# Optimization experiments

Hardware: AMD Instinct MI355X
Metric: run time of the kernel (lower is better)

Reference implementation:

```python
import jax, jax.numpy as jnp
import numpy as np

DIM = 3456      # visual_dim
E = 1024        # embed_dim = dim_head*heads = 128*8
H = 8
D = E // H
LN_EPS = 1e-5


def _mlp(x, w1, b1, w2, b2):
    # nn.Sequential(Linear, GELU(exact), Linear)
    h = jax.nn.gelu(x @ w1.T + b1, approximate=False)
    return h @ w2.T + b2


def _ln(x, g, b):
    m = jnp.mean(x, axis=-1, keepdims=True)
    v = jnp.mean((x - m) ** 2, axis=-1, keepdims=True)
    return (x - m) * jax.lax.rsqrt(v + LN_EPS) * g + b


def setup_inputs() -> dict:
    key = jax.random.key(0)
    ks = jax.random.split(key, 24)
    std = 0.02
    d = {"x": jax.random.normal(ks[0], (5, 729, DIM), dtype=jnp.float32)}
    i = 1
    for name in ("q", "k", "v"):
        d[f"{name}_w1"] = std * jax.random.normal(ks[i], (E, DIM), dtype=jnp.float32); i += 1
        d[f"{name}_b1"] = jnp.zeros((E,), jnp.float32)
        d[f"{name}_w2"] = std * jax.random.normal(ks[i], (E, E), dtype=jnp.float32); i += 1
        d[f"{name}_b2"] = jnp.zeros((E,), jnp.float32)
        d[f"ln_{name}_g"] = jnp.ones((E,), jnp.float32)
        d[f"ln_{name}_b"] = jnp.zeros((E,), jnp.float32)
    d["in_proj_w"] = std * jax.random.normal(ks[i], (3 * E, E), dtype=jnp.float32); i += 1
    d["in_proj_b"] = jnp.zeros((3 * E,), jnp.float32)
    d["out_proj_w"] = std * jax.random.normal(ks[i], (E, E), dtype=jnp.float32); i += 1
    d["out_proj_b"] = jnp.zeros((E,), jnp.float32)
    d["to_out_w"] = std * jax.random.normal(ks[i], (DIM, E), dtype=jnp.float32)
    return d


def reference(x,
              q_w1, q_b1, q_w2, q_b2, ln_q_g, ln_q_b,
              k_w1, k_b1, k_w2, k_b2, ln_k_g, ln_k_b,
              v_w1, v_b1, v_w2, v_b2, ln_v_g, ln_v_b,
              in_proj_w, in_proj_b, out_proj_w, out_proj_b, to_out_w):
    t, hw, c = x.shape
    # spatial_temporal pattern: x_multi = x, no interpolation.
    # q/k/v: MLP -> LN -> permute(1,0,2) -> divide_feature -> flatten.
    # divide_feature is a pure permutation of tokens; all tokens end up in a
    # single (L, 1, E) attention, so full attention over the flattened
    # (hw, t) token order computes the identical result.
    q = _ln(_mlp(x, q_w1, q_b1, q_w2, q_b2), ln_q_g, ln_q_b)  # (t, hw, E)
    k = _ln(_mlp(x, k_w1, k_b1, k_w2, k_b2), ln_k_g, ln_k_b)
    v = _ln(_mlp(x, v_w1, v_b1, v_w2, v_b2), ln_v_g, ln_v_b)
    L = t * hw
    q = q.transpose(1, 0, 2).reshape(L, E)  # (hw*t, E), (h,w,t)-major order
    k = k.transpose(1, 0, 2).reshape(L, E)
    v = v.transpose(1, 0, 2).reshape(L, E)
    # nn.MultiheadAttention with packed in_proj
    qp = (q @ in_proj_w[:E].T + in_proj_b[:E]).reshape(L, H, D)
    kp = (k @ in_proj_w[E:2 * E].T + in_proj_b[E:2 * E]).reshape(L, H, D)
    vp = (v @ in_proj_w[2 * E:].T + in_proj_b[2 * E:]).reshape(L, H, D)
    scale = 1.0 / jnp.sqrt(jnp.asarray(D, q.dtype))
    scores = jnp.einsum('qhd,khd->hqk', qp, kp) * scale  # (H, L, L)
    attn = jax.nn.softmax(scores, axis=-1)
    o = jnp.einsum('hqk,khd->qhd', attn, vp).reshape(L, E)
    o = o @ out_proj_w.T + out_proj_b
    o = o.reshape(hw, t, E).transpose(1, 0, 2)  # (t, hw, E)
    out = o @ to_out_w.T                         # (t, hw, c)
    return x + out
```

## Files before the change

### kernel.cpp

```cpp
#include <hip/hip_runtime.h>
#include <hip/hip_bf16.h>

#define L_TOK 3645
#define MP    3712
#define DIMV  3456
#define EDIM  1024

typedef __attribute__((ext_vector_type(8))) short bf8;
typedef __attribute__((ext_vector_type(4))) short s4v;
typedef __attribute__((ext_vector_type(4))) float f4;

__device__ __forceinline__ short f2b(float f) {
  union { float f; unsigned u; } v; v.f = f;
  unsigned r = v.u + 0x7fffu + ((v.u >> 16) & 1u);
  return (short)(r >> 16);
}
__device__ __forceinline__ float b2f(short s) {
  union { unsigned u; float f; } v; v.u = ((unsigned)(unsigned short)s) << 16;
  return v.f;
}
__device__ __forceinline__ void gld16(const void* g, void* l) {
  __builtin_amdgcn_global_load_lds(
      (const __attribute__((address_space(1))) void*)(unsigned long long)g,
      (__attribute__((address_space(3))) void*)(unsigned)(unsigned long long)l,
      16, 0, 0);
}

__global__ __launch_bounds__(256) void k_cvt(const float* __restrict__ src,
                                             short* __restrict__ dst, int n4) {
  int i = blockIdx.x * 256 + threadIdx.x;
  if (i >= n4) return;
  float4 v = ((const float4*)src)[i];
  s4v o; o[0] = f2b(v.x); o[1] = f2b(v.y); o[2] = f2b(v.z); o[3] = f2b(v.w);
  ((s4v*)dst)[i] = o;
}
__global__ __launch_bounds__(256) void k_cvt_pad(const float* __restrict__ src,
                                                 short* __restrict__ dst, int n4src, int n4tot) {
  int i = blockIdx.x * 256 + threadIdx.x;
  if (i >= n4tot) return;
  s4v o; o[0] = 0; o[1] = 0; o[2] = 0; o[3] = 0;
  if (i < n4src) {
    float4 v = ((const float4*)src)[i];
    o[0] = f2b(v.x); o[1] = f2b(v.y); o[2] = f2b(v.z); o[3] = f2b(v.w);
  }
  ((s4v*)dst)[i] = o;
}

#define GM_GELU   0
#define GM_BIAS   1
#define GM_QSCALE 2
#define GM_RESID  3

template<int MODE>
__global__ __launch_bounds__(256)
void k_gemm(const short* __restrict__ A, long sA,
            const short* __restrict__ B, long sB,
            const float* __restrict__ bias0, const float* __restrict__ bias1,
            const float* __restrict__ bias2,
            void* __restrict__ Cout, long sC,
            int N, int K, const float* __restrict__ resid)
{
  __shared__ short As[2][128 * 32];
  __shared__ short Bs[2][128 * 32];
  const int tid  = threadIdx.x;
  const int z    = blockIdx.z;

  const int nwg  = gridDim.x * gridDim.y;
  const int orig = blockIdx.y * gridDim.x + blockIdx.x;
  const int qq   = nwg >> 3, rr = nwg & 7;
  const int xcd  = orig & 7, ofs = orig >> 3;
  const int swz  = (xcd < rr ? xcd * (qq + 1) : rr * (qq + 1) + (xcd - rr) * qq) + ofs;
  const int brow = (swz / gridDim.x) * 128;
  const int bcol = (swz % gridDim.x) * 128;

  const short* Ab = A + (long)z * sA;
  const short* Bb = B + (long)z * sB;
  const float* bias = (z == 0) ? bias0 : (z == 1 ? bias1 : bias2);

  const int wave = tid >> 6, lane = tid & 63;
  const int lg = lane >> 4, lc = lane & 15;
  const int m0 = (wave >> 1) * 64, n0 = (wave & 1) * 64;

  const int r0 = tid >> 2, seg = tid & 3;
  const int r1 = r0 + 64;
  const int so0 = (seg ^ ((r0 >> 1) & 3)) * 8;
  const int so1 = (seg ^ ((r1 >> 1) & 3)) * 8;
  const short* pA0 = Ab + (long)(brow + r0) * K + so0;
  const short* pA1 = Ab + (long)(brow + r1) * K + so1;
  const short* pB0 = Bb + (long)(bcol + r0) * K + so0;
  const short* pB1 = Bb + (long)(bcol + r1) * K + so1;

  f4 acc[4][4];
  f4 zero = {0.f, 0.f, 0.f, 0.f};
#pragma unroll
  for (int i = 0; i < 4; ++i)
#pragma unroll
    for (int j = 0; j < 4; ++j) acc[i][j] = zero;

  auto STAGE = [&](int buf) {
    gld16(pA0, &As[buf][tid * 8]);
    gld16(pA1, &As[buf][(tid + 256) * 8]);
    gld16(pB0, &Bs[buf][tid * 8]);
    gld16(pB1, &Bs[buf][(tid + 256) * 8]);
    pA0 += 32; pA1 += 32; pB0 += 32; pB1 += 32;
  };

  const int NT = K >> 5;
  STAGE(0);

  for (int t = 0; t < NT; ++t) {
    const int buf = t & 1;
    asm volatile("s_waitcnt vmcnt(0)" ::: "memory");
    __builtin_amdgcn_sched_barrier(0);
    __builtin_amdgcn_s_barrier();
    if (t + 1 < NT) STAGE((t + 1) & 1);

    const short* Al = &As[buf][0];
    const short* Bl = &Bs[buf][0];
    bf8 af[4], bfr[4];
#pragma unroll
    for (int mi = 0; mi < 4; ++mi) {
      int r = m0 + mi * 16 + lc;
      af[mi] = *(const bf8*)&Al[r * 32 + ((lg ^ ((r >> 1) & 3)) * 8)];
    }
#pragma unroll
    for (int ni = 0; ni < 4; ++ni) {
      int r = n0 + ni * 16 + lc;
      bfr[ni] = *(const bf8*)&Bl[r * 32 + ((lg ^ ((r >> 1) & 3)) * 8)];
    }
    __builtin_amdgcn_s_setprio(1);
#pragma unroll
    for (int mi = 0; mi < 4; ++mi)
#pragma unroll
      for (int ni = 0; ni < 4; ++ni)
        acc[mi][ni] = __builtin_amdgcn_mfma_f32_16x16x32_bf16(af[mi], bfr[ni], acc[mi][ni], 0, 0, 0);
    __builtin_amdgcn_s_setprio(0);
    __builtin_amdgcn_sched_barrier(0);
  }

  if (MODE == GM_RESID) {
    float* C = (float*)Cout;
#pragma unroll
    for (int ni = 0; ni < 4; ++ni) {
      int col = bcol + n0 + ni * 16 + lc;
#pragma unroll
      for (int mi = 0; mi < 4; ++mi)
#pragma unroll
        for (int r = 0; r < 4; ++r) {
          int row = brow + m0 + mi * 16 + lg * 4 + r;
          if (row < L_TOK)
            C[(long)row * N + col] = acc[mi][ni][r] + resid[(long)row * N + col];
        }
    }
  } else {
    short* C = (short*)Cout + (long)z * sC;
    const float alpha = (MODE == GM_QSCALE && z == 0) ? 0.08838834764831845f : 1.0f;
#pragma unroll
    for (int ni = 0; ni < 4; ++ni) {
      int col = bcol + n0 + ni * 16 + lc;
      float bv = bias[col];
#pragma unroll
      for (int mi = 0; mi < 4; ++mi)
#pragma unroll
        for (int r = 0; r < 4; ++r) {
          int row = brow + m0 + mi * 16 + lg * 4 + r;
          float v = acc[mi][ni][r] + bv;
          if (MODE == GM_GELU) v = 0.5f * v * (1.f + erff(v * 0.70710678118654752f));
          v *= alpha;
          C[(long)row * EDIM + col] = f2b(v);
        }
    }
  }
}

__global__ __launch_bounds__(256)
void k_ln(const short* __restrict__ A, short* __restrict__ Y,
          const float* __restrict__ g0, const float* __restrict__ g1, const float* __restrict__ g2,
          const float* __restrict__ b0, const float* __restrict__ b1, const float* __restrict__ b2)
{
  const int row = blockIdx.x, z = blockIdx.y;
  const float* g = (z == 0) ? g0 : (z == 1 ? g1 : g2);
  const float* b = (z == 0) ? b0 : (z == 1 ? b1 : b2);
  const short* a = A + ((long)z * MP + row) * EDIM;
  short* y = Y + ((long)z * MP + row) * EDIM;
  const int t = threadIdx.x;
  s4v v = *(const s4v*)&a[t * 4];
  float x0 = b2f(v[0]), x1 = b2f(v[1]), x2 = b2f(v[2]), x3 = b2f(v[3]);
  float s = x0 + x1 + x2 + x3;
  float q = x0 * x0 + x1 * x1 + x2 * x2 + x3 * x3;
#pragma unroll
  for (int off = 1; off < 64; off <<= 1) { s += __shfl_xor(s, off); q += __shfl_xor(q, off); }
  __shared__ float rs[4], rq[4];
  if ((t & 63) == 0) { rs[t >> 6] = s; rq[t >> 6] = q; }
  __syncthreads();
  s = rs[0] + rs[1] + rs[2] + rs[3];
  q = rq[0] + rq[1] + rq[2] + rq[3];
  float mean = s * (1.f / 1024.f);
  float var  = q * (1.f / 1024.f) - mean * mean;
  float rstd = rsqrtf(var + 1e-5f);
  s4v o;
#pragma unroll
  for (int j = 0; j < 4; ++j) {
    int col = t * 4 + j;
    o[j] = f2b((b2f(v[j]) - mean) * rstd * g[col] + b[col]);
  }
  *(s4v*)&y[t * 4] = o;
}

__global__ __launch_bounds__(256)
void k_vtrans(const short* __restrict__ vp, short* __restrict__ vpT)
{
  const int kb = blockIdx.x * 64, h = blockIdx.y;
  __shared__ short T[64 * 128];
  const int tid = threadIdx.x;
#pragma unroll
  for (int i = 0; i < 4; ++i) {
    int c = tid + 256 * i;
    int r = c >> 4, x = c & 15;
    bf8 val = *(const bf8*)&vp[(long)(kb + r) * EDIM + h * 128 + x * 8];
    *(bf8*)&T[r * 128 + ((x ^ (r & 7)) * 8)] = val;
  }
  __syncthreads();
#pragma unroll
  for (int i = 0; i < 4; ++i) {
    int c = tid + 256 * i;
    int dr = c >> 3, x = c & 7;
    short tmp[8];
#pragma unroll
    for (int e = 0; e < 8; ++e) {
      int kv = x * 8 + e;
      tmp[e] = T[kv * 128 + (((dr >> 3) ^ (kv & 7)) << 3) + (dr & 7)];
    }
    *(bf8*)&vpT[((long)h * 128 + dr) * MP + kb + x * 8] = *(bf8*)tmp;
  }
}

__global__ __launch_bounds__(256)
void k_attn(const short* __restrict__ qp, const short* __restrict__ kp,
            const short* __restrict__ vpT, short* __restrict__ o)
{
  const int bx = blockIdx.x;
  const int h = bx & 7, qb = (bx >> 3) * 128;
  const int tid = threadIdx.x, wave = tid >> 6, lane = tid & 63;
  const int lg = lane >> 4, lc = lane & 15;
  __shared__ short Ks[2][64 * 128];
  __shared__ short Vs[2][128 * 64];
  __shared__ short Ps[4][32 * 64];

  const int q0 = qb + wave * 32;
  bf8 qf[2][4];
#pragma unroll
  for (int g = 0; g < 2; ++g)
#pragma unroll
    for (int d4 = 0; d4 < 4; ++d4)
      qf[g][d4] = *(const bf8*)&qp[(long)(q0 + g * 16 + lc) * EDIM + h * 128 + d4 * 32 + lg * 8];

  f4 oacc[2][8];
  f4 zero = {0.f, 0.f, 0.f, 0.f};
#pragma unroll
  for (int g = 0; g < 2; ++g)
#pragma unroll
    for (int dt = 0; dt < 8; ++dt) oacc[g][dt] = zero;
  float lsum0 = 0.f, lsum1 = 0.f;

  auto STAGE = [&](short* ksb, short* vsb, int kb) {
#pragma unroll
    for (int i = 0; i < 4; ++i) {
      int c = tid + 256 * i; int r = c >> 4, x = c & 15;
      gld16(&kp[(long)(kb + r) * EDIM + h * 128 + (x ^ (r & 7)) * 8], &ksb[c * 8]);
    }
#pragma unroll
    for (int i = 0; i < 4; ++i) {
      int c = tid + 256 * i; int dr = c >> 3, x = c & 7;
      gld16(&vpT[((long)h * 128 + dr) * MP + kb + (x ^ (dr & 7)) * 8], &vsb[c * 8]);
    }
  };

  const int NTILE = (L_TOK + 63) / 64;
  STAGE(Ks[0], Vs[0], 0);

  for (int t = 0; t < NTILE; ++t) {
    const int kb = t * 64;
    const short* ksb = Ks[t & 1];
    const short* vsb = Vs[t & 1];
    __builtin_amdgcn_s_barrier();
    if (t + 1 < NTILE) {
      STAGE(Ks[(t + 1) & 1], Vs[(t + 1) & 1], kb + 64);
      asm volatile("s_waitcnt vmcnt(8)" ::: "memory");
    } else {
      asm volatile("s_waitcnt vmcnt(0)" ::: "memory");
    }
    __builtin_amdgcn_sched_barrier(0);
    __builtin_amdgcn_s_barrier();
    __builtin_amdgcn_sched_barrier(0);

#pragma unroll
    for (int s = 0; s < 4; ++s) {
      const int krow = s * 16 + lc;
      bf8 kf[4];
#pragma unroll
      for (int d4 = 0; d4 < 4; ++d4)
        kf[d4] = *(const bf8*)&ksb[krow * 128 + (((d4 * 4 + lg) ^ (krow & 7)) * 8)];
      f4 sa0 = zero, sa1 = zero;
      __builtin_amdgcn_s_setprio(1);
#pragma unroll
      for (int d4 = 0; d4 < 4; ++d4) {
        sa0 = __builtin_amdgcn_mfma_f32_16x16x32_bf16(kf[d4], qf[0][d4], sa0, 0, 0, 0);
        sa1 = __builtin_amdgcn_mfma_f32_16x16x32_bf16(kf[d4], qf[1][d4], sa1, 0, 0, 0);
      }
      __builtin_amdgcn_s_setprio(0);
      const int kvb = kb + s * 16 + lg * 4;
#pragma unroll
      for (int g = 0; g < 2; ++g) {
        f4 sa = g ? sa1 : sa0;
        float p[4];
#pragma unroll
        for (int r = 0; r < 4; ++r) {
          float e = __expf(sa[r]);
          p[r] = (kvb + r < L_TOK) ? e : 0.f;
          if (g) lsum1 += p[r]; else lsum0 += p[r];
        }
        s4v pk; pk[0] = f2b(p[0]); pk[1] = f2b(p[1]); pk[2] = f2b(p[2]); pk[3] = f2b(p[3]);
        *(s4v*)&Ps[wave][(g * 16 + lc) * 64 + ((s * 16 + lg * 4) ^ ((lc & 7) << 3))] = pk;
      }
    }
    bf8 pf[2][2];
#pragma unroll
    for (int g = 0; g < 2; ++g) {
      pf[g][0] = *(const bf8*)&Ps[wave][(g * 16 + lc) * 64 + ((lg * 8) ^ ((lc & 7) << 3))];
      pf[g][1] = *(const bf8*)&Ps[wave][(g * 16 + lc) * 64 + ((32 + lg * 8) ^ ((lc & 7) << 3))];
    }
#pragma unroll
    for (int dt = 0; dt < 8; ++dt) {
      const int vrow = dt * 16 + lc;
      bf8 vf0 = *(const bf8*)&vsb[vrow * 64 + ((lg ^ (vrow & 7)) * 8)];
      bf8 vf1 = *(const bf8*)&vsb[vrow * 64 + (((4 + lg) ^ (vrow & 7)) * 8)];
      __builtin_amdgcn_s_setprio(1);
      oacc[0][dt] = __builtin_amdgcn_mfma_f32_16x16x32_bf16(pf[0][0], vf0, oacc[0][dt], 0, 0, 0);
      oacc[0][dt] = __builtin_amdgcn_mfma_f32_16x16x32_bf16(pf[0][1], vf1, oacc[0][dt], 0, 0, 0);
      oacc[1][dt] = __builtin_amdgcn_mfma_f32_16x16x32_bf16(pf[1][0], vf0, oacc[1][dt], 0, 0, 0);
      oacc[1][dt] = __builtin_amdgcn_mfma_f32_16x16x32_bf16(pf[1][1], vf1, oacc[1][dt], 0, 0, 0);
      __builtin_amdgcn_s_setprio(0);
    }
    __builtin_amdgcn_sched_barrier(0);
  }

  lsum0 += __shfl_xor(lsum0, 16);
  lsum0 += __shfl_xor(lsum0, 32);
  lsum1 += __shfl_xor(lsum1, 16);
  lsum1 += __shfl_xor(lsum1, 32);
#pragma unroll
  for (int g = 0; g < 2; ++g) {
    float ls = g ? lsum1 : lsum0;
    float rinv[4];
#pragma unroll
    for (int r = 0; r < 4; ++r) rinv[r] = 1.f / __shfl(ls, lg * 4 + r);
#pragma unroll
    for (int dt = 0; dt < 8; ++dt)
#pragma unroll
      for (int r = 0; r < 4; ++r) {
        int orow = q0 + g * 16 + lg * 4 + r;
        o[(long)orow * EDIM + h * 128 + dt * 16 + lc] = f2b(oacc[g][dt][r] * rinv[r]);
      }
  }
}

extern "C" void kernel_launch(void* const* d_in, const int* in_sizes, int n_in,
                              void* d_out, int out_size, void* d_ws, size_t ws_size,
                              hipStream_t stream)
{
  const float* x   = (const float*)d_in[0];
  const float* ipb = (const float*)d_in[20];
  const float* opb = (const float*)d_in[22];

  char* ws = (char*)d_ws;
  short* regA = (short*)(ws + 0);
  short* regB = (short*)(ws + 25657344);
  short* w1b  = (short*)(ws + 48463872);
  short* w2b  = (short*)(ws + 69697536);
  short* wpb  = (short*)(ws + 75988992);
  short* wob  = (short*)(ws + 82280448);
  short* wtb  = (short*)(ws + 84377600);
  short* vpT  = (short*)(ws + 91455488);

  short* xb  = regA;
  short* h1  = regB;
  short* aln = regA;
  short* lnq = regB;
  short* proj = regA;
  short* ob  = regB;
  short* o2  = (short*)(ws + 25657344 + 7602176);

  k_cvt_pad<<<12528, 256, 0, stream>>>(x, xb, 3149280, 3207168);
  k_cvt<<<3456, 256, 0, stream>>>((const float*)d_in[1],  w1b,            884736);
  k_cvt<<<3456, 256, 0, stream>>>((const float*)d_in[7],  w1b + 3538944,  884736);
  k_cvt<<<3456, 256, 0, stream>>>((const float*)d_in[13], w1b + 7077888,  884736);
  k_cvt<<<1024, 256, 0, stream>>>((const float*)d_in[3],  w2b,            262144);
  k_cvt<<<1024, 256, 0, stream>>>((const float*)d_in[9],  w2b + 1048576,  262144);
  k_cvt<<<1024, 256, 0, stream>>>((const float*)d_in[15], w2b + 2097152,  262144);
  k_cvt<<<3072, 256, 0, stream>>>((const float*)d_in[19], wpb,            786432);
  k_cvt<<<1024, 256, 0, stream>>>((const float*)d_in[21], wob,            262144);
  k_cvt<<<3456, 256, 0, stream>>>((const float*)d_in[23], wtb,            884736);

  dim3 g3(8, 29, 3), g1(8, 29, 1);
  k_gemm<GM_GELU><<<g3, 256, 0, stream>>>(xb, 0, w1b, 3538944,
      (const float*)d_in[2], (const float*)d_in[8], (const float*)d_in[14],
      h1, (long)MP * EDIM, EDIM, DIMV, nullptr);
  k_gemm<GM_BIAS><<<g3, 256, 0, stream>>>(h1, (long)MP * EDIM, w2b, 1048576,
      (const float*)d_in[4], (const float*)d_in[10], (const float*)d_in[16],
      aln, (long)MP * EDIM, EDIM, EDIM, nullptr);
  dim3 gl(MP, 3);
  k_ln<<<gl, 256, 0, stream>>>(aln, lnq,
      (const float*)d_in[5], (const float*)d_in[11], (const float*)d_in[17],
      (const float*)d_in[6], (const float*)d_in[12], (const float*)d_in[18]);
  k_gemm<GM_QSCALE><<<g3, 256, 0, stream>>>(lnq, (long)MP * EDIM, wpb, 1048576,
      ipb, ipb + 1024, ipb + 2048,
      proj, (long)MP * EDIM, EDIM, EDIM, nullptr);
  dim3 gt(MP / 64, 8);
  k_vtrans<<<gt, 256, 0, stream>>>(proj + 2L * MP * EDIM, vpT);
  k_attn<<<(MP / 128) * 8, 256, 0, stream>>>(proj, proj + (long)MP * EDIM, vpT, ob);
  k_gemm<GM_BIAS><<<g1, 256, 0, stream>>>(ob, 0, wob, 0,
      opb, opb, opb, o2, 0, EDIM, EDIM, nullptr);
  dim3 g5(27, 29, 1);
  k_gemm<GM_RESID><<<g5, 256, 0, stream>>>(o2, 0, wtb, 0,
      nullptr, nullptr, nullptr, d_out, 0, DIMV, EDIM, x);
}
```

Before: 421.6 us.

## Use 256x256 GEMM tiles with 512 threads and split attention over keys

Result: slower. 452.1 us (+7.2%).

```diff
diff --git a/kernel.cpp b/kernel.cpp
--- a/kernel.cpp
+++ b/kernel.cpp
@@ -52,6 +52,153 @@
 #define GM_RESID  3
 
 template<int MODE>
+__global__ __launch_bounds__(512, 2)
+void k_gemm2(const short* __restrict__ A, long sA,
+             const short* __restrict__ B, long sB,
+             const float* __restrict__ bias0, const float* __restrict__ bias1,
+             const float* __restrict__ bias2,
+             void* __restrict__ Cout, long sC,
+             int N, int K, const float* __restrict__ resid)
+{
+  __shared__ short L[2][2][2][8192];
+  const int tid = threadIdx.x;
+  const int z = blockIdx.z;
+  const int brow = blockIdx.y * 256;
+  const int bcol = blockIdx.x * 256;
+  const short* Ab = A + (long)z * sA;
+  const short* Bb = B + (long)z * sB;
+  const float* bias = (z == 0) ? bias0 : (z == 1 ? bias1 : bias2);
+
+  const int wave = tid >> 6, lane = tid & 63;
+  const int lg = lane >> 4, lc = lane & 15;
+  const int wm = wave >> 2, wn = wave & 3;
+
+  const int r0 = tid >> 3, x0 = tid & 7;
+  const int c1 = tid + 512;
+  const int r1 = c1 >> 3, x1 = c1 & 7;
+  const short* pa[2][2];
+  const short* pb[2][2];
+#pragma unroll
+  for (int half = 0; half < 2; ++half) {
+    int ra0 = brow + half * 128 + r0; if (ra0 > MP - 1) ra0 = MP - 1;
+    int ra1 = brow + half * 128 + r1; if (ra1 > MP - 1) ra1 = MP - 1;
+    int rb0 = bcol + half * 128 + r0; if (rb0 > N - 1) rb0 = N - 1;
+    int rb1 = bcol + half * 128 + r1; if (rb1 > N - 1) rb1 = N - 1;
+    pa[half][0] = Ab + (long)ra0 * K + ((x0 ^ (r0 & 7)) * 8);
+    pa[half][1] = Ab + (long)ra1 * K + ((x1 ^ (r1 & 7)) * 8);
+    pb[half][0] = Bb + (long)rb0 * K + ((x0 ^ (r0 & 7)) * 8);
+    pb[half][1] = Bb + (long)rb1 * K + ((x1 ^ (r1 & 7)) * 8);
+  }
+
+  f4 acc[8][4];
+  f4 zero = {0.f, 0.f, 0.f, 0.f};
+#pragma unroll
+  for (int i = 0; i < 8; ++i)
+#pragma unroll
+    for (int j = 0; j < 4; ++j) acc[i][j] = zero;
+
+  auto STG = [&](int bufi, int ab, int half) {
+    if (ab == 0) {
+      gld16(pa[half][0], &L[bufi][0][half][tid * 8]);
+      gld16(pa[half][1], &L[bufi][0][half][c1 * 8]);
+      pa[half][0] += 64; pa[half][1] += 64;
+    } else {
+      gld16(pb[half][0], &L[bufi][1][half][tid * 8]);
+      gld16(pb[half][1], &L[bufi][1][half][c1 * 8]);
+      pb[half][0] += 64; pb[half][1] += 64;
+    }
+  };
+
+  const int NT = K >> 6;
+  STG(0, 0, 0); STG(0, 0, 1); STG(0, 1, 0); STG(0, 1, 1);
+
+  const int bhalf = wn >> 1, brw = (wn & 1) * 64;
+  bf8 bfr[4][2];
+
+  for (int kt = 0; kt < NT; ++kt) {
+    const int buf = kt & 1, nb = buf ^ 1;
+    const bool more = (kt + 1 < NT);
+#pragma unroll
+    for (int p = 0; p < 4; ++p) {
+      if (p == 0) {
+        if (more) { STG(nb, 0, 0); asm volatile("s_waitcnt vmcnt(2)" ::: "memory"); }
+        else      { asm volatile("s_waitcnt vmcnt(0)" ::: "memory"); }
+        __builtin_amdgcn_sched_barrier(0);
+        __builtin_amdgcn_s_barrier();
+        __builtin_amdgcn_sched_barrier(0);
+#pragma unroll
+        for (int nf = 0; nf < 4; ++nf)
+#pragma unroll
+          for (int ks = 0; ks < 2; ++ks) {
+            int row = brw + nf * 16 + lc;
+            int seg = (ks * 4 + lg) ^ (row & 7);
+            bfr[nf][ks] = *(const bf8*)&L[buf][1][bhalf][row * 64 + seg * 8];
+          }
+      } else {
+        if (more) STG(nb, p >> 1, p & 1);
+      }
+      bf8 af[2][2];
+#pragma unroll
+      for (int m2 = 0; m2 < 2; ++m2)
+#pragma unroll
+        for (int ks = 0; ks < 2; ++ks) {
+          int row = p * 32 + m2 * 16 + lc;
+          int seg = (ks * 4 + lg) ^ (row & 7);
+          af[m2][ks] = *(const bf8*)&L[buf][0][wm][row * 64 + seg * 8];
+        }
+      asm volatile("s_waitcnt lgkmcnt(0)" ::: "memory");
+      __builtin_amdgcn_sched_barrier(0);
+      __builtin_amdgcn_s_setprio(1);
+#pragma unroll
+      for (int m2 = 0; m2 < 2; ++m2)
+#pragma unroll
+        for (int nf = 0; nf < 4; ++nf)
+#pragma unroll
+          for (int ks = 0; ks < 2; ++ks)
+            acc[p * 2 + m2][nf] = __builtin_amdgcn_mfma_f32_16x16x32_bf16(
+                af[m2][ks], bfr[nf][ks], acc[p * 2 + m2][nf], 0, 0, 0);
+      __builtin_amdgcn_s_setprio(0);
+      __builtin_amdgcn_sched_barrier(0);
+      __builtin_amdgcn_s_barrier();
+    }
+  }
+
+  if (MODE == GM_RESID) {
+    float* C = (float*)Cout;
+#pragma unroll
+    for (int nf = 0; nf < 4; ++nf) {
+      int col = bcol + wn * 64 + nf * 16 + lc;
+#pragma unroll
+      for (int mf = 0; mf < 8; ++mf)
+#pragma unroll
+        for (int r = 0; r < 4; ++r) {
+          int row = brow + wm * 128 + mf * 16 + lg * 4 + r;
+          if (row < L_TOK && col < N)
+            C[(long)row * N + col] = acc[mf][nf][r] + resid[(long)row * N + col];
+        }
+    }
+  } else {
+    short* C = (short*)Cout + (long)z * sC;
+    const float alpha = (MODE == GM_QSCALE && z == 0) ? 0.08838834764831845f : 1.0f;
+#pragma unroll
+    for (int nf = 0; nf < 4; ++nf) {
+      int col = bcol + wn * 64 + nf * 16 + lc;
+      float bv = bias[col];
+#pragma unroll
+      for (int mf = 0; mf < 8; ++mf)
+#pragma unroll
+        for (int r = 0; r < 4; ++r) {
+          int row = brow + wm * 128 + mf * 16 + lg * 4 + r;
+          float v = acc[mf][nf][r] + bv;
+          if (MODE == GM_GELU) v = 0.5f * v * (1.f + erff(v * 0.70710678118654752f));
+          v *= alpha;
+          if (row < MP) C[(long)row * EDIM + col] = f2b(v);
+        }
+    }
+  }
+}
+
+template<int MODE>
 __global__ __launch_bounds__(256)
 void k_gemm(const short* __restrict__ A, long sA,
             const short* __restrict__ B, long sB,
@@ -64,7 +211,6 @@
   __shared__ short Bs[2][128 * 32];
   const int tid  = threadIdx.x;
   const int z    = blockIdx.z;
-
   const int nwg  = gridDim.x * gridDim.y;
   const int orig = blockIdx.y * gridDim.x + blockIdx.x;
   const int qq   = nwg >> 3, rr = nwg & 7;
@@ -107,14 +253,12 @@
 
   const int NT = K >> 5;
   STAGE(0);
-
   for (int t = 0; t < NT; ++t) {
     const int buf = t & 1;
     asm volatile("s_waitcnt vmcnt(0)" ::: "memory");
     __builtin_amdgcn_sched_barrier(0);
     __builtin_amdgcn_s_barrier();
     if (t + 1 < NT) STAGE((t + 1) & 1);
-
     const short* Al = &As[buf][0];
     const short* Bl = &Bs[buf][0];
     bf8 af[4], bfr[4];
@@ -237,10 +381,18 @@
 
 __global__ __launch_bounds__(256)
 void k_attn(const short* __restrict__ qp, const short* __restrict__ kp,
-            const short* __restrict__ vpT, short* __restrict__ o)
+            const short* __restrict__ vpT,
+            short* __restrict__ op0, short* __restrict__ op1,
+            float* __restrict__ lsums)
 {
   const int bx = blockIdx.x;
-  const int h = bx & 7, qb = (bx >> 3) * 128;
+  const int h = bx & 7;
+  const int t2 = bx >> 3;
+  const int qi = t2 % 29, sp = t2 / 29;
+  const int qb = qi * 128;
+  short* opart = sp ? op1 : op0;
+  const int t0 = sp ? 29 : 0, t1 = sp ? 57 : 29;
+
   const int tid = threadIdx.x, wave = tid >> 6, lane = tid & 63;
   const int lg = lane >> 4, lc = lane & 15;
   __shared__ short Ks[2][64 * 128];
@@ -276,15 +428,14 @@
     }
   };
 
-  const int NTILE = (L_TOK + 63) / 64;
-  STAGE(Ks[0], Vs[0], 0);
-
-  for (int t = 0; t < NTILE; ++t) {
+  STAGE(Ks[t0 & 1], Vs[t0 & 1], t0 * 64);
+
+  for (int t = t0; t < t1; ++t) {
     const int kb = t * 64;
     const short* ksb = Ks[t & 1];
     const short* vsb = Vs[t & 1];
     __builtin_amdgcn_s_barrier();
-    if (t + 1 < NTILE) {
+    if (t + 1 < t1) {
       STAGE(Ks[(t + 1) & 1], Vs[(t + 1) & 1], kb + 64);
       asm volatile("s_waitcnt vmcnt(8)" ::: "memory");
     } else {
@@ -349,20 +500,35 @@
   lsum0 += __shfl_xor(lsum0, 32);
   lsum1 += __shfl_xor(lsum1, 16);
   lsum1 += __shfl_xor(lsum1, 32);
-#pragma unroll
-  for (int g = 0; g < 2; ++g) {
-    float ls = g ? lsum1 : lsum0;
-    float rinv[4];
-#pragma unroll
-    for (int r = 0; r < 4; ++r) rinv[r] = 1.f / __shfl(ls, lg * 4 + r);
+  if (lg == 0) {
+    lsums[((sp * 8) + h) * MP + q0 + lc]      = lsum0;
+    lsums[((sp * 8) + h) * MP + q0 + 16 + lc] = lsum1;
+  }
+#pragma unroll
+  for (int g = 0; g < 2; ++g)
 #pragma unroll
     for (int dt = 0; dt < 8; ++dt)
 #pragma unroll
       for (int r = 0; r < 4; ++r) {
         int orow = q0 + g * 16 + lg * 4 + r;
-        o[(long)orow * EDIM + h * 128 + dt * 16 + lc] = f2b(oacc[g][dt][r] * rinv[r]);
+        opart[(long)orow * EDIM + h * 128 + dt * 16 + lc] = f2b(oacc[g][dt][r]);
       }
-  }
+}
+
+__global__ __launch_bounds__(256)
+void k_comb(const short* __restrict__ p0, const short* __restrict__ p1,
+            const float* __restrict__ ls, short* __restrict__ ob)
+{
+  int i = blockIdx.x * 256 + threadIdx.x;
+  int q = i >> 7;
+  int h = (i & 127) >> 4;
+  float rinv = 1.f / (ls[h * MP + q] + ls[(8 + h) * MP + q]);
+  bf8 a = ((const bf8*)p0)[i];
+  bf8 b = ((const bf8*)p1)[i];
+  bf8 o;
+#pragma unroll
+  for (int j = 0; j < 8; ++j) o[j] = f2b((b2f(a[j]) + b2f(b[j])) * rinv);
+  ((bf8*)ob)[i] = o;
 }
 
 extern "C" void kernel_launch(void* const* d_in, const int* in_sizes, int n_in,
@@ -389,7 +555,10 @@
   short* lnq = regB;
   short* proj = regA;
   short* ob  = regB;
-  short* o2  = (short*)(ws + 25657344 + 7602176);
+  short* o2  = (short*)(ws + 33259520);
+  short* pt1 = o2;
+  short* pt0 = (short*)(ws + 40861696);
+  float* lsums = (float*)(ws + 22806528);
 
   k_cvt_pad<<<12528, 256, 0, stream>>>(x, xb, 3149280, 3207168);
   k_cvt<<<3456, 256, 0, stream>>>((const float*)d_in[1],  w1b,            884736);
@@ -402,26 +571,29 @@
   k_cvt<<<1024, 256, 0, stream>>>((const float*)d_in[21], wob,            262144);
   k_cvt<<<3456, 256, 0, stream>>>((const float*)d_in[23], wtb,            884736);
 
-  dim3 g3(8, 29, 3), g1(8, 29, 1);
-  k_gemm<GM_GELU><<<g3, 256, 0, stream>>>(xb, 0, w1b, 3538944,
+  dim3 gg3(4, 15, 3);
+  k_gemm2<GM_GELU><<<gg3, 512, 0, stream>>>(xb, 0, w1b, 3538944,
       (const float*)d_in[2], (const float*)d_in[8], (const float*)d_in[14],
       h1, (long)MP * EDIM, EDIM, DIMV, nullptr);
-  k_gemm<GM_BIAS><<<g3, 256, 0, stream>>>(h1, (long)MP * EDIM, w2b, 1048576,
+  k_gemm2<GM_BIAS><<<gg3, 512, 0, stream>>>(h1, (long)MP * EDIM, w2b, 1048576,
       (const float*)d_in[4], (const float*)d_in[10], (const float*)d_in[16],
       aln, (long)MP * EDIM, EDIM, EDIM, nullptr);
   dim3 gl(MP, 3);
   k_ln<<<gl, 256, 0, stream>>>(aln, lnq,
       (const float*)d_in[5], (const float*)d_in[11], (const float*)d_in[17],
       (const float*)d_in[6], (const float*)d_in[12], (const float*)d_in[18]);
-  k_gemm<GM_QSCALE><<<g3, 256, 0, stream>>>(lnq, (long)MP * EDIM, wpb, 1048576,
+  k_gemm2<GM_QSCALE><<<gg3, 512, 0, stream>>>(lnq, (long)MP * EDIM, wpb, 1048576,
       ipb, ipb + 1024, ipb + 2048,
       proj, (long)MP * EDIM, EDIM, EDIM, nullptr);
   dim3 gt(MP / 64, 8);
   k_vtrans<<<gt, 256, 0, stream>>>(proj + 2L * MP * EDIM, vpT);
-  k_attn<<<(MP / 128) * 8, 256, 0, stream>>>(proj, proj + (long)MP * EDIM, vpT, ob);
+  k_attn<<<29 * 2 * 8, 256, 0, stream>>>(proj, proj + (long)MP * EDIM, vpT,
+      pt0, pt1, lsums);
+  k_comb<<<(MP * EDIM / 8) / 256, 256, 0, stream>>>(pt0, pt1, lsums, ob);
+  dim3 g1(8, 29, 1);
   k_gemm<GM_BIAS><<<g1, 256, 0, stream>>>(ob, 0, wob, 0,
       opb, opb, opb, o2, 0, EDIM, EDIM, nullptr);
-  dim3 g5(27, 29, 1);
-  k_gemm<GM_RESID><<<g5, 256, 0, stream>>>(o2, 0, wtb, 0,
+  dim3 gg5(14, 15, 1);
+  k_gemm2<GM_RESID><<<gg5, 512, 0, stream>>>(o2, 0, wtb, 0,
       nullptr, nullptr, nullptr, d_out, 0, DIMV, EDIM, x);
 }
```

## Fold out_proj into to_out weight and split attention over keys in two

Applied to the files above, without the earlier changes.

New measurement: 420.5 us. About the same (-0.3%).

```diff
diff --git a/kernel.cpp b/kernel.cpp
--- a/kernel.cpp
+++ b/kernel.cpp
@@ -45,11 +45,41 @@
   }
   ((s4v*)dst)[i] = o;
 }
+__global__ __launch_bounds__(256)
+void k_cvt_t(const float* __restrict__ src, short* __restrict__ dst, int n) {
+  __shared__ float T[64][65];
+  const int bi = blockIdx.x * 64, bj = blockIdx.y * 64;
+  const int tx = threadIdx.x & 63, ty = threadIdx.x >> 6;
+#pragma unroll
+  for (int r = 0; r < 64; r += 4)
+    T[r + ty][tx] = src[(long)(bj + r + ty) * n + bi + tx];
+  __syncthreads();
+#pragma unroll
+  for (int r = 0; r < 64; r += 4)
+    dst[(long)(bi + r + ty) * n + bj + tx] = f2b(T[tx][r + ty]);
+}
+__global__ __launch_bounds__(256)
+void k_bvec(const float* __restrict__ wt, const float* __restrict__ opb,
+            float* __restrict__ bp) {
+  const int n = blockIdx.x * 4 + (threadIdx.x >> 6);
+  const int lane = threadIdx.x & 63;
+  const float* row = wt + (long)n * 1024;
+  float s = 0.f;
+  for (int k = lane * 4; k < 1024; k += 256) {
+    float4 w = *(const float4*)&row[k];
+    float4 b = *(const float4*)&opb[k];
+    s += w.x * b.x + w.y * b.y + w.z * b.z + w.w * b.w;
+  }
+#pragma unroll
+  for (int off = 1; off < 64; off <<= 1) s += __shfl_xor(s, off);
+  if (lane == 0) bp[n] = s;
+}
 
 #define GM_GELU   0
 #define GM_BIAS   1
 #define GM_QSCALE 2
 #define GM_RESID  3
+#define GM_PLAIN  4
 
 template<int MODE>
 __global__ __launch_bounds__(256)
@@ -64,7 +94,6 @@
   __shared__ short Bs[2][128 * 32];
   const int tid  = threadIdx.x;
   const int z    = blockIdx.z;
-
   const int nwg  = gridDim.x * gridDim.y;
   const int orig = blockIdx.y * gridDim.x + blockIdx.x;
   const int qq   = nwg >> 3, rr = nwg & 7;
@@ -107,14 +136,12 @@
 
   const int NT = K >> 5;
   STAGE(0);
-
   for (int t = 0; t < NT; ++t) {
     const int buf = t & 1;
     asm volatile("s_waitcnt vmcnt(0)" ::: "memory");
     __builtin_amdgcn_sched_barrier(0);
     __builtin_amdgcn_s_barrier();
     if (t + 1 < NT) STAGE((t + 1) & 1);
-
     const short* Al = &As[buf][0];
     const short* Bl = &Bs[buf][0];
     bf8 af[4], bfr[4];
@@ -143,13 +170,14 @@
 #pragma unroll
     for (int ni = 0; ni < 4; ++ni) {
       int col = bcol + n0 + ni * 16 + lc;
+      float bv = bias[col];
 #pragma unroll
       for (int mi = 0; mi < 4; ++mi)
 #pragma unroll
         for (int r = 0; r < 4; ++r) {
           int row = brow + m0 + mi * 16 + lg * 4 + r;
           if (row < L_TOK)
-            C[(long)row * N + col] = acc[mi][ni][r] + resid[(long)row * N + col];
+            C[(long)row * N + col] = acc[mi][ni][r] + bv + resid[(long)row * N + col];
         }
     }
   } else {
@@ -158,7 +186,8 @@
 #pragma unroll
     for (int ni = 0; ni < 4; ++ni) {
       int col = bcol + n0 + ni * 16 + lc;
-      float bv = bias[col];
+      float bv = 0.f;
+      if (MODE != GM_PLAIN) bv = bias[col];
 #pragma unroll
       for (int mi = 0; mi < 4; ++mi)
 #pragma unroll
@@ -237,10 +266,18 @@
 
 __global__ __launch_bounds__(256)
 void k_attn(const short* __restrict__ qp, const short* __restrict__ kp,
-            const short* __restrict__ vpT, short* __restrict__ o)
+            const short* __restrict__ vpT,
+            short* __restrict__ op0, short* __restrict__ op1,
+            float* __restrict__ lsums)
 {
   const int bx = blockIdx.x;
-  const int h = bx & 7, qb = (bx >> 3) * 128;
+  const int h = bx & 7;
+  const int t2 = bx >> 3;
+  const int qi = t2 % 29, sp = t2 / 29;
+  const int qb = qi * 128;
+  short* opart = sp ? op1 : op0;
+  const int t0 = sp ? 29 : 0, t1 = sp ? 57 : 29;
+
   const int tid = threadIdx.x, wave = tid >> 6, lane = tid & 63;
   const int lg = lane >> 4, lc = lane & 15;
   __shared__ short Ks[2][64 * 128];
@@ -276,15 +313,14 @@
     }
   };
 
-  const int NTILE = (L_TOK + 63) / 64;
-  STAGE(Ks[0], Vs[0], 0);
-
-  for (int t = 0; t < NTILE; ++t) {
+  STAGE(Ks[t0 & 1], Vs[t0 & 1], t0 * 64);
+
+  for (int t = t0; t < t1; ++t) {
     const int kb = t * 64;
     const short* ksb = Ks[t & 1];
     const short* vsb = Vs[t & 1];
     __builtin_amdgcn_s_barrier();
-    if (t + 1 < NTILE) {
+    if (t + 1 < t1) {
       STAGE(Ks[(t + 1) & 1], Vs[(t + 1) & 1], kb + 64);
       asm volatile("s_waitcnt vmcnt(8)" ::: "memory");
     } else {
@@ -349,20 +385,35 @@
   lsum0 += __shfl_xor(lsum0, 32);
   lsum1 += __shfl_xor(lsum1, 16);
   lsum1 += __shfl_xor(lsum1, 32);
-#pragma unroll
-  for (int g = 0; g < 2; ++g) {
-    float ls = g ? lsum1 : lsum0;
-    float rinv[4];
-#pragma unroll
-    for (int r = 0; r < 4; ++r) rinv[r] = 1.f / __shfl(ls, lg * 4 + r);
+  if (lg == 0) {
+    lsums[((sp * 8) + h) * MP + q0 + lc]      = lsum0;
+    lsums[((sp * 8) + h) * MP + q0 + 16 + lc] = lsum1;
+  }
+#pragma unroll
+  for (int g = 0; g < 2; ++g)
 #pragma unroll
     for (int dt = 0; dt < 8; ++dt)
 #pragma unroll
       for (int r = 0; r < 4; ++r) {
         int orow = q0 + g * 16 + lg * 4 + r;
-        o[(long)orow * EDIM + h * 128 + dt * 16 + lc] = f2b(oacc[g][dt][r] * rinv[r]);
+        opart[(long)orow * EDIM + h * 128 + dt * 16 + lc] = f2b(oacc[g][dt][r]);
       }
-  }
+}
+
+__global__ __launch_bounds__(256)
+void k_comb(const short* __restrict__ p0, const short* __restrict__ p1,
+            const float* __restrict__ ls, short* __restrict__ ob)
+{
+  int i = blockIdx.x * 256 + threadIdx.x;
+  int q = i >> 7;
+  int h = (i & 127) >> 4;
+  float rinv = 1.f / (ls[h * MP + q] + ls[(8 + h) * MP + q]);
+  bf8 a = ((const bf8*)p0)[i];
+  bf8 b = ((const bf8*)p1)[i];
+  bf8 o;
+#pragma unroll
+  for (int j = 0; j < 8; ++j) o[j] = f2b((b2f(a[j]) + b2f(b[j])) * rinv);
+  ((bf8*)ob)[i] = o;
 }
 
 extern "C" void kernel_launch(void* const* d_in, const int* in_sizes, int n_in,
@@ -379,7 +430,7 @@
   short* w1b  = (short*)(ws + 48463872);
   short* w2b  = (short*)(ws + 69697536);
   short* wpb  = (short*)(ws + 75988992);
-  short* wob  = (short*)(ws + 82280448);
+  short* woT  = (short*)(ws + 82280448);
   short* wtb  = (short*)(ws + 84377600);
   short* vpT  = (short*)(ws + 91455488);
 
@@ -389,7 +440,11 @@
   short* lnq = regB;
   short* proj = regA;
   short* ob  = regB;
-  short* o2  = (short*)(ws + 25657344 + 7602176);
+  short* pt1 = (short*)(ws + 33259520);
+  short* pt0 = (short*)(ws + 40861696);
+  float* lsums = (float*)(ws + 22806528);
+  float* bp    = (float*)(ws + 23068672);
+  short* wprime = w1b;
 
   k_cvt_pad<<<12528, 256, 0, stream>>>(x, xb, 3149280, 3207168);
   k_cvt<<<3456, 256, 0, stream>>>((const float*)d_in[1],  w1b,            884736);
@@ -399,13 +454,18 @@
   k_cvt<<<1024, 256, 0, stream>>>((const float*)d_in[9],  w2b + 1048576,  262144);
   k_cvt<<<1024, 256, 0, stream>>>((const float*)d_in[15], w2b + 2097152,  262144);
   k_cvt<<<3072, 256, 0, stream>>>((const float*)d_in[19], wpb,            786432);
-  k_cvt<<<1024, 256, 0, stream>>>((const float*)d_in[21], wob,            262144);
   k_cvt<<<3456, 256, 0, stream>>>((const float*)d_in[23], wtb,            884736);
+  dim3 gct(16, 16);
+  k_cvt_t<<<gct, 256, 0, stream>>>((const float*)d_in[21], woT, 1024);
 
   dim3 g3(8, 29, 3), g1(8, 29, 1);
   k_gemm<GM_GELU><<<g3, 256, 0, stream>>>(xb, 0, w1b, 3538944,
       (const float*)d_in[2], (const float*)d_in[8], (const float*)d_in[14],
       h1, (long)MP * EDIM, EDIM, DIMV, nullptr);
+  k_bvec<<<864, 256, 0, stream>>>((const float*)d_in[23], opb, bp);
+  dim3 gwp(8, 27, 1);
+  k_gemm<GM_PLAIN><<<gwp, 256, 0, stream>>>(wtb, 0, woT, 0,
+      nullptr, nullptr, nullptr, wprime, 0, EDIM, EDIM, nullptr);
   k_gemm<GM_BIAS><<<g3, 256, 0, stream>>>(h1, (long)MP * EDIM, w2b, 1048576,
       (const float*)d_in[4], (const float*)d_in[10], (const float*)d_in[16],
       aln, (long)MP * EDIM, EDIM, EDIM, nullptr);
@@ -418,10 +478,10 @@
       proj, (long)MP * EDIM, EDIM, EDIM, nullptr);
   dim3 gt(MP / 64, 8);
   k_vtrans<<<gt, 256, 0, stream>>>(proj + 2L * MP * EDIM, vpT);
-  k_attn<<<(MP / 128) * 8, 256, 0, stream>>>(proj, proj + (long)MP * EDIM, vpT, ob);
-  k_gemm<GM_BIAS><<<g1, 256, 0, stream>>>(ob, 0, wob, 0,
-      opb, opb, opb, o2, 0, EDIM, EDIM, nullptr);
+  k_attn<<<29 * 2 * 8, 256, 0, stream>>>(proj, proj + (long)MP * EDIM, vpT,
+      pt0, pt1, lsums);
+  k_comb<<<(MP * EDIM / 8) / 256, 256, 0, stream>>>(pt0, pt1, lsums, ob);
   dim3 g5(27, 29, 1);
-  k_gemm<GM_RESID><<<g5, 256, 0, stream>>>(o2, 0, wtb, 0,
-      nullptr, nullptr, nullptr, d_out, 0, DIMV, EDIM, x);
-}
+  k_gemm<GM_RESID><<<g5, 256, 0, stream>>>(ob, 0, wprime, 0,
+      bp, bp, bp, d_out, 0, DIMV, EDIM, x);
+}
```
